# Kernel optimization log

Measured on AMD Instinct MI355X. Metric: run time of the kernel, lower is better.

Reference implementation:

```python
import jax, jax.numpy as jnp
import numpy as np

T = 0.5  # sharpening temperature
M, N, DK, DV = 8192, 8192, 512, 512


def setup_inputs() -> dict:
    key = jax.random.key(0)
    kq, kk, kv = jax.random.split(key, 3)
    Q = jax.random.normal(kq, (M, DK), dtype=jnp.float32)
    K = jax.random.normal(kk, (N, DK), dtype=jnp.float32)
    V = jax.random.normal(kv, (N, DV), dtype=jnp.float32)
    return {"Q": Q, "K": K, "V": V}


def reference(Q, K, V):
    d_k = K.shape[1]
    scores = jnp.matmul(Q, K.T) / np.sqrt(d_k)          # (m, n)
    attn = jax.nn.softmax(scores, axis=-1)              # (m, n)
    # sharpen: p^(1/T), renormalize over keys (dim=1 for 2D == last axis)
    u = jnp.power(attn, 1.0 / T)
    attn = u / jnp.sum(u, axis=1, keepdims=True)
    return jnp.matmul(attn, V)                          # (m, d_v)
```

## Files before the change

### kernel.cpp

```cpp
#include <hip/hip_runtime.h>

typedef unsigned short u16;
typedef __attribute__((ext_vector_type(8))) short bf16x8;
typedef __attribute__((ext_vector_type(4))) float f32x4;
typedef __attribute__((ext_vector_type(4))) u16 u16x4;

#define MFMA16(a, b, c) __builtin_amdgcn_mfma_f32_16x16x32_bf16(a, b, c, 0, 0, 0)

__device__ __forceinline__ u16 f2bf(float f) {
    union { float f; unsigned u; } v; v.f = f;
    unsigned r = (v.u + 0x7FFFu + ((v.u >> 16) & 1u)) >> 16;
    return (u16)r;
}

__device__ __forceinline__ void gload_lds16(const void* g, void* l) {
    __builtin_amdgcn_global_load_lds((const __attribute__((address_space(1))) void*)g,
                                     (__attribute__((address_space(3))) void*)l, 16, 0, 0);
}

__global__ __launch_bounds__(256) void cvt_kernel(const float* __restrict__ src,
                                                  u16* __restrict__ dst, int n4, float scale) {
    int i = blockIdx.x * 256 + threadIdx.x;
    if (i >= n4) return;
    f32x4 v = *(const f32x4*)(src + (size_t)i * 4);
    u16x4 o;
#pragma unroll
    for (int j = 0; j < 4; ++j) o[j] = f2bf(v[j] * scale);
    *(u16x4*)(dst + (size_t)i * 4) = o;
}

__global__ __launch_bounds__(256) void prep_vt(const float* __restrict__ V, u16* __restrict__ Vt) {
    __shared__ float tile[64][65];
    int t = threadIdx.x;
    int n0 = blockIdx.x * 64;
    int d0 = blockIdx.y * 64;
    int tr = t >> 4, tc = t & 15;
#pragma unroll
    for (int p = 0; p < 4; ++p) {
        int n = p * 16 + tr;
        f32x4 v = *(const f32x4*)(V + (size_t)(n0 + n) * 512 + d0 + tc * 4);
#pragma unroll
        for (int j = 0; j < 4; ++j) tile[n][tc * 4 + j] = v[j];
    }
    __syncthreads();
#pragma unroll
    for (int p = 0; p < 4; ++p) {
        int d = p * 16 + tr;
        u16x4 o;
#pragma unroll
        for (int j = 0; j < 4; ++j) o[j] = f2bf(tile[tc * 4 + j][d]);
        *(u16x4*)(Vt + (size_t)(d0 + d) * 8192 + n0 + tc * 4) = o;
    }
}

__global__ __launch_bounds__(512) void flash_kernel(
    const u16* __restrict__ Qs, const u16* __restrict__ Kb, const u16* __restrict__ Vt,
    float* __restrict__ Opart, float* __restrict__ lpart) {
    __shared__ __align__(16) u16 lds_k[2][64 * 512];
    __shared__ __align__(16) u16 lds_p[2][64 * 64];
    __shared__ float s_l[2][64];

    const int tid = threadIdx.x;
    const int wid = tid >> 6;
    const int lane = tid & 63;
    const int lo = lane & 15;
    const int hi = lane >> 4;
    const int mi = wid >> 1;
    const int nj = wid & 1;

    const int bx = blockIdx.x;
    const int x = bx & 7;
    const int g = bx >> 3;
    const int ks = x >> 2;
    const int mtile = g * 4 + (x & 3);
    const int key0 = ks * 4096;

    bf16x8 qf[16];
    {
        const u16* qrow = Qs + (size_t)(mtile * 64 + mi * 16 + lo) * 512 + hi * 8;
#pragma unroll
        for (int kt = 0; kt < 16; ++kt) qf[kt] = *(const bf16x8*)(qrow + kt * 32);
    }

    f32x4 o[4][4];
#pragma unroll
    for (int a = 0; a < 4; ++a)
#pragma unroll
        for (int b = 0; b < 4; ++b) o[a][b] = (f32x4){0.f, 0.f, 0.f, 0.f};
    float lsum = 0.f;
    bf16x8 vb[4][2];

    const int cbase = ((hi ^ (lo & 3)) + ((lo >> 2) & 1) * 4) * 8;
    const int rowA = (nj * 32 + lo) * 512;

    const int qrow = mi * 16 + lo;
    const int ch0 = ((nj * 4 + (hi >> 1)) ^ (qrow & 7));
    const int ch1 = ((nj * 4 + 2 + (hi >> 1)) ^ (qrow & 7));
    const int pw0 = qrow * 64 + (ch0 << 3) + (hi & 1) * 4;
    const int pw1 = qrow * 64 + (ch1 << 3) + (hi & 1) * 4;

#define STAGE_K(IT, BUF)                                                            \
    {                                                                               \
        const u16* kb_ = Kb + (size_t)(key0 + (IT) * 64) * 512;                     \
        _Pragma("unroll") for (int r8_ = 0; r8_ < 8; ++r8_) {                       \
            int row_ = (wid << 3) + r8_;                                            \
            gload_lds16(kb_ + (size_t)row_ * 512 + ((lane ^ (row_ & 7)) << 3),      \
                        &lds_k[BUF][row_ * 512]);                                   \
        }                                                                           \
    }

#define S_COMPUTE(BUF, S0, S1)                                                      \
    {                                                                               \
        const u16* kb = &lds_k[BUF][0];                                             \
        const u16* pAe = kb + rowA + cbase;                                         \
        const u16* pAo = kb + rowA + (cbase ^ 32);                                  \
        const u16* pBe = pAe + 16 * 512;                                            \
        const u16* pBo = pAo + 16 * 512;                                            \
        _Pragma("unroll") for (int kt2 = 0; kt2 < 8; ++kt2) {                       \
            bf16x8 ae = *(const bf16x8*)(pAe + kt2 * 64);                           \
            bf16x8 be = *(const bf16x8*)(pBe + kt2 * 64);                           \
            bf16x8 ao = *(const bf16x8*)(pAo + kt2 * 64);                           \
            bf16x8 bo = *(const bf16x8*)(pBo + kt2 * 64);                           \
            S0 = MFMA16(ae, qf[2 * kt2], S0);                                       \
            S1 = MFMA16(be, qf[2 * kt2], S1);                                       \
            S0 = MFMA16(ao, qf[2 * kt2 + 1], S0);                                   \
            S1 = MFMA16(bo, qf[2 * kt2 + 1], S1);                                   \
        }                                                                           \
    }

#define PV_STEP(PBUF)                                                               \
    {                                                                               \
        _Pragma("unroll") for (int mt = 0; mt < 4; ++mt) {                          \
            int m = mt * 16 + lo;                                                   \
            int c0 = hi ^ (m & 7);                                                  \
            int c1 = (4 + hi) ^ (m & 7);                                            \
            bf16x8 pa0 = *(const bf16x8*)(&lds_p[PBUF][m * 64 + c0 * 8]);           \
            bf16x8 pa1 = *(const bf16x8*)(&lds_p[PBUF][m * 64 + c1 * 8]);           \
            _Pragma("unroll") for (int nt = 0; nt < 4; ++nt) {                      \
                f32x4 c_ = o[mt][nt];                                               \
                c_ = MFMA16(pa0, vb[nt][0], c_);                                    \
                c_ = MFMA16(pa1, vb[nt][1], c_);                                    \
                o[mt][nt] = c_;                                                     \
            }                                                                       \
        }                                                                           \
    }

#define EXP_PW(S0, S1, PBUF)                                                        \
    {                                                                               \
        u16x4 w0, w1;                                                               \
        _Pragma("unroll") for (int r = 0; r < 4; ++r) {                             \
            float p0 = __expf((S0)[r]);                                             \
            float p1 = __expf((S1)[r]);                                             \
            lsum += p0 + p1;                                                        \
            w0[r] = f2bf(p0);                                                       \
            w1[r] = f2bf(p1);                                                       \
        }                                                                           \
        *(u16x4*)(&lds_p[PBUF][pw0]) = w0;                                          \
        *(u16x4*)(&lds_p[PBUF][pw1]) = w1;                                          \
    }

#define VB_LOAD(T)                                                                  \
    {                                                                               \
        _Pragma("unroll") for (int nt = 0; nt < 4; ++nt) {                          \
            const u16* vrow = Vt + (size_t)(wid * 64 + nt * 16 + lo) * 8192 +       \
                              key0 + (T) * 64 + hi * 8;                             \
            vb[nt][0] = *(const bf16x8*)(vrow);                                     \
            vb[nt][1] = *(const bf16x8*)(vrow + 32);                                \
        }                                                                           \
    }

    STAGE_K(0, 0)
    asm volatile("s_waitcnt vmcnt(0)\n\ts_barrier" ::: "memory");

    {
        STAGE_K(1, 1)
        f32x4 s0 = {0.f, 0.f, 0.f, 0.f}, s1 = {0.f, 0.f, 0.f, 0.f};
        __builtin_amdgcn_s_setprio(1);
        S_COMPUTE(0, s0, s1)
        __builtin_amdgcn_s_setprio(0);
        EXP_PW(s0, s1, 0)
        VB_LOAD(0)
        asm volatile("s_waitcnt vmcnt(0) lgkmcnt(0)\n\ts_barrier" ::: "memory");
    }

    for (int t = 1; t < 64; ++t) {
        const int cur = t & 1;
        if (t < 63) STAGE_K(t + 1, cur ^ 1)
        f32x4 s0 = {0.f, 0.f, 0.f, 0.f}, s1 = {0.f, 0.f, 0.f, 0.f};
        __builtin_amdgcn_s_setprio(1);
        S_COMPUTE(cur, s0, s1)
        PV_STEP(cur ^ 1)
        __builtin_amdgcn_s_setprio(0);
        EXP_PW(s0, s1, cur)
        VB_LOAD(t)
        asm volatile("s_waitcnt vmcnt(0) lgkmcnt(0)\n\ts_barrier" ::: "memory");
    }

    __builtin_amdgcn_s_setprio(1);
    PV_STEP(1)
    __builtin_amdgcn_s_setprio(0);

    lsum += __shfl_xor(lsum, 16);
    lsum += __shfl_xor(lsum, 32);
    if (lane < 16) s_l[nj][qrow] = lsum;
    __syncthreads();

    const int lb = mtile * 2 + ks;
    {
        float* Ob = Opart + (size_t)lb * (64 * 512);
#pragma unroll
        for (int mt = 0; mt < 4; ++mt)
#pragma unroll
            for (int nt = 0; nt < 4; ++nt)
#pragma unroll
                for (int r = 0; r < 4; ++r) {
                    int row = mt * 16 + hi * 4 + r;
                    int col = wid * 64 + nt * 16 + lo;
                    Ob[row * 512 + col] = o[mt][nt][r];
                }
        if (tid < 64) {
            lpart[lb * 64 + tid] = s_l[0][tid] + s_l[1][tid];
        }
    }
}

__global__ __launch_bounds__(256) void combine_kernel(const float* __restrict__ Opart,
                                                      const float* __restrict__ lpart,
                                                      float* __restrict__ out) {
    int i = blockIdx.x * 256 + threadIdx.x;
    int row = i >> 7;
    int c4 = i & 127;
    int mtile = row >> 6, rl = row & 63;
    int b0 = mtile * 2, b1 = b0 + 1;
    float inv = 1.0f / (lpart[b0 * 64 + rl] + lpart[b1 * 64 + rl]);
    f32x4 a = *(const f32x4*)(Opart + (size_t)b0 * 32768 + rl * 512 + c4 * 4);
    f32x4 b = *(const f32x4*)(Opart + (size_t)b1 * 32768 + rl * 512 + c4 * 4);
    f32x4 r = (a + b) * inv;
    *(f32x4*)(out + (size_t)row * 512 + c4 * 4) = r;
}

extern "C" void kernel_launch(void* const* d_in, const int* in_sizes, int n_in,
                              void* d_out, int out_size, void* d_ws, size_t ws_size,
                              hipStream_t stream) {
    const float* Q = (const float*)d_in[0];
    const float* K = (const float*)d_in[1];
    const float* V = (const float*)d_in[2];
    float* out = (float*)d_out;
    char* ws = (char*)d_ws;

    u16* Qs = (u16*)(ws + 0);
    u16* Kb = (u16*)(ws + 8388608);
    u16* Vt = (u16*)(ws + 16777216);
    float* Op = (float*)(ws + 25165824);
    float* lp = (float*)(ws + 58720256);

    const float scale = 0.08838834764831845f;
    cvt_kernel<<<4096, 256, 0, stream>>>(Q, Qs, 1048576, scale);
    cvt_kernel<<<4096, 256, 0, stream>>>(K, Kb, 1048576, 1.0f);
    prep_vt<<<dim3(128, 8), 256, 0, stream>>>(V, Vt);
    flash_kernel<<<256, 512, 0, stream>>>(Qs, Kb, Vt, Op, lp);
    combine_kernel<<<4096, 256, 0, stream>>>(Op, lp, out);
}
```

Baseline: 256.4 us.

## Split QK^T reduction across wave pairs and drop software-pipelined PV

Each wave now computes a 32x32 score block over half of the head dimension, so every K fragment read from LDS feeds two Q row tiles. Partial scores are exchanged through a new LDS scratch buffer and summed before the exponential. The previous one-step skew between S and PV (double-buffered P) is removed. PV now runs in the same iteration after an extra barrier, trading lower LDS read traffic for more barriers and less overlap.

New measurement: 278.1 us. 1.08x slower.

```diff
diff --git a/kernel.cpp b/kernel.cpp
--- a/kernel.cpp
+++ b/kernel.cpp
@@ -57,7 +57,8 @@
     const u16* __restrict__ Qs, const u16* __restrict__ Kb, const u16* __restrict__ Vt,
     float* __restrict__ Opart, float* __restrict__ lpart) {
     __shared__ __align__(16) u16 lds_k[2][64 * 512];
-    __shared__ __align__(16) u16 lds_p[2][64 * 64];
+    __shared__ __align__(16) u16 lds_p[64 * 64];
+    __shared__ __align__(16) float lds_sx[16 * 256];
     __shared__ float s_l[2][64];
 
     const int tid = threadIdx.x;
@@ -65,8 +66,9 @@
     const int lane = tid & 63;
     const int lo = lane & 15;
     const int hi = lane >> 4;
-    const int mi = wid >> 1;
-    const int nj = wid & 1;
+    const int kh = wid & 1;
+    const int nj = (wid >> 1) & 1;
+    const int rs = wid >> 2;
 
     const int bx = blockIdx.x;
     const int x = bx & 7;
@@ -75,11 +77,13 @@
     const int mtile = g * 4 + (x & 3);
     const int key0 = ks * 4096;
 
-    bf16x8 qf[16];
-    {
-        const u16* qrow = Qs + (size_t)(mtile * 64 + mi * 16 + lo) * 512 + hi * 8;
-#pragma unroll
-        for (int kt = 0; kt < 16; ++kt) qf[kt] = *(const bf16x8*)(qrow + kt * 32);
+    bf16x8 qf[2][8];
+#pragma unroll
+    for (int rt = 0; rt < 2; ++rt) {
+        const u16* qrow =
+            Qs + (size_t)(mtile * 64 + rs * 32 + rt * 16 + lo) * 512 + kh * 256 + hi * 8;
+#pragma unroll
+        for (int j = 0; j < 8; ++j) qf[rt][j] = *(const bf16x8*)(qrow + j * 32);
     }
 
     f32x4 o[4][4];
@@ -92,12 +96,14 @@
 
     const int cbase = ((hi ^ (lo & 3)) + ((lo >> 2) & 1) * 4) * 8;
     const int rowA = (nj * 32 + lo) * 512;
-
-    const int qrow = mi * 16 + lo;
-    const int ch0 = ((nj * 4 + (hi >> 1)) ^ (qrow & 7));
-    const int ch1 = ((nj * 4 + 2 + (hi >> 1)) ^ (qrow & 7));
-    const int pw0 = qrow * 64 + (ch0 << 3) + (hi & 1) * 4;
-    const int pw1 = qrow * 64 + (ch1 << 3) + (hi & 1) * 4;
+    const int khofs = kh * 256;
+
+    const int prow = rs * 32 + kh * 16 + lo;
+    const int pw0 = prow * 64 + ((((nj << 2) + (hi >> 1)) ^ (prow & 7)) << 3) + (hi & 1) * 4;
+    const int pw1 = prow * 64 + ((((nj << 2) + 2 + (hi >> 1)) ^ (prow & 7)) << 3) + (hi & 1) * 4;
+
+    const int sxw = (wid * 2) * 256 + lane * 4;
+    const int sxr = ((wid ^ 1) * 2) * 256 + lane * 4;
 
 #define STAGE_K(IT, BUF)                                                            \
     {                                                                               \
@@ -109,33 +115,37 @@
         }                                                                           \
     }
 
-#define S_COMPUTE(BUF, S0, S1)                                                      \
+#define S_COMPUTE(BUF)                                                              \
     {                                                                               \
         const u16* kb = &lds_k[BUF][0];                                             \
-        const u16* pAe = kb + rowA + cbase;                                         \
-        const u16* pAo = kb + rowA + (cbase ^ 32);                                  \
-        const u16* pBe = pAe + 16 * 512;                                            \
-        const u16* pBo = pAo + 16 * 512;                                            \
-        _Pragma("unroll") for (int kt2 = 0; kt2 < 8; ++kt2) {                       \
-            bf16x8 ae = *(const bf16x8*)(pAe + kt2 * 64);                           \
-            bf16x8 be = *(const bf16x8*)(pBe + kt2 * 64);                           \
-            bf16x8 ao = *(const bf16x8*)(pAo + kt2 * 64);                           \
-            bf16x8 bo = *(const bf16x8*)(pBo + kt2 * 64);                           \
-            S0 = MFMA16(ae, qf[2 * kt2], S0);                                       \
-            S1 = MFMA16(be, qf[2 * kt2], S1);                                       \
-            S0 = MFMA16(ao, qf[2 * kt2 + 1], S0);                                   \
-            S1 = MFMA16(bo, qf[2 * kt2 + 1], S1);                                   \
-        }                                                                           \
-    }
-
-#define PV_STEP(PBUF)                                                               \
+        const u16* p0e = kb + rowA + khofs + cbase;                                 \
+        const u16* p0o = kb + rowA + khofs + (cbase ^ 32);                          \
+        const u16* p1e = p0e + 16 * 512;                                            \
+        const u16* p1o = p0o + 16 * 512;                                            \
+        _Pragma("unroll") for (int kt2 = 0; kt2 < 4; ++kt2) {                       \
+            bf16x8 a0e = *(const bf16x8*)(p0e + kt2 * 64);                          \
+            bf16x8 a1e = *(const bf16x8*)(p1e + kt2 * 64);                          \
+            bf16x8 a0o = *(const bf16x8*)(p0o + kt2 * 64);                          \
+            bf16x8 a1o = *(const bf16x8*)(p1o + kt2 * 64);                          \
+            s00 = MFMA16(a0e, qf[0][2 * kt2], s00);                                 \
+            s10 = MFMA16(a0e, qf[1][2 * kt2], s10);                                 \
+            s01 = MFMA16(a1e, qf[0][2 * kt2], s01);                                 \
+            s11 = MFMA16(a1e, qf[1][2 * kt2], s11);                                 \
+            s00 = MFMA16(a0o, qf[0][2 * kt2 + 1], s00);                             \
+            s10 = MFMA16(a0o, qf[1][2 * kt2 + 1], s10);                             \
+            s01 = MFMA16(a1o, qf[0][2 * kt2 + 1], s01);                             \
+            s11 = MFMA16(a1o, qf[1][2 * kt2 + 1], s11);                             \
+        }                                                                           \
+    }
+
+#define PV_STEP                                                                     \
     {                                                                               \
         _Pragma("unroll") for (int mt = 0; mt < 4; ++mt) {                          \
             int m = mt * 16 + lo;                                                   \
             int c0 = hi ^ (m & 7);                                                  \
             int c1 = (4 + hi) ^ (m & 7);                                            \
-            bf16x8 pa0 = *(const bf16x8*)(&lds_p[PBUF][m * 64 + c0 * 8]);           \
-            bf16x8 pa1 = *(const bf16x8*)(&lds_p[PBUF][m * 64 + c1 * 8]);           \
+            bf16x8 pa0 = *(const bf16x8*)(&lds_p[m * 64 + c0 * 8]);                 \
+            bf16x8 pa1 = *(const bf16x8*)(&lds_p[m * 64 + c1 * 8]);                 \
             _Pragma("unroll") for (int nt = 0; nt < 4; ++nt) {                      \
                 f32x4 c_ = o[mt][nt];                                               \
                 c_ = MFMA16(pa0, vb[nt][0], c_);                                    \
@@ -145,20 +155,6 @@
         }                                                                           \
     }
 
-#define EXP_PW(S0, S1, PBUF)                                                        \
-    {                                                                               \
-        u16x4 w0, w1;                                                               \
-        _Pragma("unroll") for (int r = 0; r < 4; ++r) {                             \
-            float p0 = __expf((S0)[r]);                                             \
-            float p1 = __expf((S1)[r]);                                             \
-            lsum += p0 + p1;                                                        \
-            w0[r] = f2bf(p0);                                                       \
-            w1[r] = f2bf(p1);                                                       \
-        }                                                                           \
-        *(u16x4*)(&lds_p[PBUF][pw0]) = w0;                                          \
-        *(u16x4*)(&lds_p[PBUF][pw1]) = w1;                                          \
-    }
-
 #define VB_LOAD(T)                                                                  \
     {                                                                               \
         _Pragma("unroll") for (int nt = 0; nt < 4; ++nt) {                          \
@@ -172,37 +168,48 @@
     STAGE_K(0, 0)
     asm volatile("s_waitcnt vmcnt(0)\n\ts_barrier" ::: "memory");
 
-    {
-        STAGE_K(1, 1)
-        f32x4 s0 = {0.f, 0.f, 0.f, 0.f}, s1 = {0.f, 0.f, 0.f, 0.f};
+    for (int t = 0; t < 64; ++t) {
+        const int cur = t & 1;
+        VB_LOAD(t)
+        asm volatile("" ::: "memory");
+        if (t < 63) STAGE_K(t + 1, cur ^ 1)
+
+        f32x4 s00 = {0.f, 0.f, 0.f, 0.f}, s01 = s00, s10 = s00, s11 = s00;
         __builtin_amdgcn_s_setprio(1);
-        S_COMPUTE(0, s0, s1)
+        S_COMPUTE(cur)
         __builtin_amdgcn_s_setprio(0);
-        EXP_PW(s0, s1, 0)
-        VB_LOAD(0)
-        asm volatile("s_waitcnt vmcnt(0) lgkmcnt(0)\n\ts_barrier" ::: "memory");
-    }
-
-    for (int t = 1; t < 64; ++t) {
-        const int cur = t & 1;
-        if (t < 63) STAGE_K(t + 1, cur ^ 1)
-        f32x4 s0 = {0.f, 0.f, 0.f, 0.f}, s1 = {0.f, 0.f, 0.f, 0.f};
+
+        *(f32x4*)(&lds_sx[sxw]) = kh ? s00 : s10;
+        *(f32x4*)(&lds_sx[sxw + 256]) = kh ? s01 : s11;
+        asm volatile("s_waitcnt lgkmcnt(0)\n\ts_barrier" ::: "memory");
+
+        {
+            f32x4 fA = (kh ? s10 : s00) + *(const f32x4*)(&lds_sx[sxr]);
+            f32x4 fB = (kh ? s11 : s01) + *(const f32x4*)(&lds_sx[sxr + 256]);
+            u16x4 w0, w1;
+#pragma unroll
+            for (int r = 0; r < 4; ++r) {
+                float p0 = __expf(fA[r]);
+                float p1 = __expf(fB[r]);
+                lsum += p0 + p1;
+                w0[r] = f2bf(p0);
+                w1[r] = f2bf(p1);
+            }
+            *(u16x4*)(&lds_p[pw0]) = w0;
+            *(u16x4*)(&lds_p[pw1]) = w1;
+        }
+        asm volatile("s_waitcnt lgkmcnt(0)\n\ts_barrier" ::: "memory");
+
         __builtin_amdgcn_s_setprio(1);
-        S_COMPUTE(cur, s0, s1)
-        PV_STEP(cur ^ 1)
+        PV_STEP
         __builtin_amdgcn_s_setprio(0);
-        EXP_PW(s0, s1, cur)
-        VB_LOAD(t)
-        asm volatile("s_waitcnt vmcnt(0) lgkmcnt(0)\n\ts_barrier" ::: "memory");
-    }
-
-    __builtin_amdgcn_s_setprio(1);
-    PV_STEP(1)
-    __builtin_amdgcn_s_setprio(0);
+
+        if (t < 63) asm volatile("s_waitcnt vmcnt(0)\n\ts_barrier" ::: "memory");
+    }
 
     lsum += __shfl_xor(lsum, 16);
     lsum += __shfl_xor(lsum, 32);
-    if (lane < 16) s_l[nj][qrow] = lsum;
+    if (lane < 16) s_l[nj][rs * 32 + kh * 16 + lo] = lsum;
     __syncthreads();
 
     const int lb = mtile * 2 + ks;
```
